# Optimization experiments

Measured on AMD Instinct MI355X. Metric: run time of the kernel, lower is better.

The kernel has to match this reference:

```python
import jax, jax.numpy as jnp
import numpy as np

N = 100000
E = 625000
IN_C, HID_C, OUT_C = 128, 128, 128


def setup_inputs() -> dict:
    key = jax.random.key(0)
    ks = jax.random.split(key, 8)
    x = jax.random.normal(ks[0], (N, IN_C), dtype=jnp.float32)
    edge_index = jax.random.randint(ks[1], (2, E), 0, N, dtype=jnp.int64)
    # SAGEConv layer 1: lin_l (on aggregated neighbors, with bias), lin_r (on root, no bias)
    s1 = 1.0 / np.sqrt(IN_C)
    W1l = jax.random.uniform(ks[2], (HID_C, IN_C), minval=-s1, maxval=s1, dtype=jnp.float32)
    b1l = jax.random.uniform(ks[3], (HID_C,), minval=-s1, maxval=s1, dtype=jnp.float32)
    W1r = jax.random.uniform(ks[4], (HID_C, IN_C), minval=-s1, maxval=s1, dtype=jnp.float32)
    s2 = 1.0 / np.sqrt(HID_C)
    W2l = jax.random.uniform(ks[5], (OUT_C, HID_C), minval=-s2, maxval=s2, dtype=jnp.float32)
    b2l = jax.random.uniform(ks[6], (OUT_C,), minval=-s2, maxval=s2, dtype=jnp.float32)
    W2r = jax.random.uniform(ks[7], (OUT_C, HID_C), minval=-s2, maxval=s2, dtype=jnp.float32)
    return {"x": x, "edge_index": edge_index,
            "W1l": W1l, "b1l": b1l, "W1r": W1r,
            "W2l": W2l, "b2l": b2l, "W2r": W2r}


def _sage_conv(x, src, dst, Wl, bl, Wr, num_nodes):
    # mean aggregation of source features into destination nodes
    agg = jax.ops.segment_sum(x[src], dst, num_segments=num_nodes)  # [N, d]
    cnt = jax.ops.segment_sum(jnp.ones((src.shape[0],), dtype=x.dtype), dst,
                              num_segments=num_nodes)  # [N]
    mean = agg / jnp.maximum(cnt, 1.0)[:, None]  # zero-degree nodes stay 0
    return mean @ Wl.T + bl + x @ Wr.T


def reference(x, edge_index, W1l, b1l, W1r, W2l, b2l, W2r):
    src, dst = edge_index[0], edge_index[1]
    h = jax.nn.sigmoid(_sage_conv(x, src, dst, W1l, b1l, W1r, N))
    out = _sage_conv(h, src, dst, W2l, b2l, W2r, N)
    return out
```

## Files before the change

kernel.cpp:

```cpp
#include <hip/hip_runtime.h>
#include <math.h>

#define NN 100000
#define NE 625000
#define CC 128
#define CAP 32
#define NT 3125

typedef __attribute__((ext_vector_type(8))) short bf16x8;
typedef __attribute__((ext_vector_type(4))) float f32x4;

__device__ __forceinline__ unsigned short f2b(float f) {
    unsigned int u = __float_as_uint(f);
    unsigned int r = (u + 0x7FFFu + ((u >> 16) & 1u)) >> 16;
    return (unsigned short)r;
}
__device__ __forceinline__ float b2f(unsigned int h) {
    return __uint_as_float(h << 16);
}


__global__ void build_kernel(const int* __restrict__ src, const int* __restrict__ dst,
                             int* __restrict__ cnt, int* __restrict__ col) {
    int e = blockIdx.x * blockDim.x + threadIdx.x;
    if (e < NE) {
        int d = dst[e];
        int p = atomicAdd(&cnt[d], 1);
        if (p < CAP) col[d * CAP + p] = src[e];
    }
}


__global__ __launch_bounds__(256) void cvtX_kernel(const float* __restrict__ x,
                                                   unsigned short* __restrict__ xb) {
    size_t i = ((size_t)blockIdx.x * 256 + threadIdx.x) * 4;
    float4 v = *(const float4*)&x[i];
    ushort2 lo = { f2b(v.x), f2b(v.y) };
    ushort2 hi = { f2b(v.z), f2b(v.w) };
    *(ushort2*)&xb[i]     = lo;
    *(ushort2*)&xb[i + 2] = hi;
}


__global__ void cvtW_kernel(const float* __restrict__ W1l, const float* __restrict__ W1r,
                            const float* __restrict__ W2l, const float* __restrict__ W2r,
                            unsigned short* __restrict__ Wcat1,
                            unsigned short* __restrict__ Wcat2) {
    int i = blockIdx.x * blockDim.x + threadIdx.x;
    int layer = i >> 15;
    int local = i & 32767;
    int c = local >> 8;
    int k = local & 255;
    const float* Wl = layer ? W2l : W1l;
    const float* Wr = layer ? W2r : W1r;
    float v = (k < CC) ? Wl[c * CC + k] : Wr[c * CC + (k - CC)];
    (layer ? Wcat2 : Wcat1)[local] = f2b(v);
}


__global__ __launch_bounds__(256) void gather_kernel(const unsigned short* __restrict__ feat,
                                                     const int* __restrict__ cnt,
                                                     const int* __restrict__ col,
                                                     unsigned short* __restrict__ aggb) {
    int gtid = blockIdx.x * blockDim.x + threadIdx.x;
    int node = gtid >> 6;
    if (node >= NN) return;
    int lane = gtid & 63;
    int g    = lane >> 4;
    int c8   = (lane & 15) * 8;
    int deg  = cnt[node];
    int dmin = deg < CAP ? deg : CAP;
    const int* bucket = col + node * CAP;
    float s0 = 0, s1 = 0, s2 = 0, s3 = 0, s4 = 0, s5 = 0, s6 = 0, s7 = 0;
    for (int j = g; j < dmin; j += 4) {
        int s = bucket[j];
        uint4 u = *(const uint4*)&feat[(size_t)s * CC + c8];
        s0 += b2f(u.x & 0xFFFFu); s1 += b2f(u.x >> 16);
        s2 += b2f(u.y & 0xFFFFu); s3 += b2f(u.y >> 16);
        s4 += b2f(u.z & 0xFFFFu); s5 += b2f(u.z >> 16);
        s6 += b2f(u.w & 0xFFFFu); s7 += b2f(u.w >> 16);
    }
    s0 += __shfl_xor(s0, 16); s0 += __shfl_xor(s0, 32);
    s1 += __shfl_xor(s1, 16); s1 += __shfl_xor(s1, 32);
    s2 += __shfl_xor(s2, 16); s2 += __shfl_xor(s2, 32);
    s3 += __shfl_xor(s3, 16); s3 += __shfl_xor(s3, 32);
    s4 += __shfl_xor(s4, 16); s4 += __shfl_xor(s4, 32);
    s5 += __shfl_xor(s5, 16); s5 += __shfl_xor(s5, 32);
    s6 += __shfl_xor(s6, 16); s6 += __shfl_xor(s6, 32);
    s7 += __shfl_xor(s7, 16); s7 += __shfl_xor(s7, 32);
    if (g == 0) {
        float iv = 1.0f / (float)(deg > 0 ? deg : 1);
        uint4 o;
        o.x = (unsigned int)f2b(s0 * iv) | ((unsigned int)f2b(s1 * iv) << 16);
        o.y = (unsigned int)f2b(s2 * iv) | ((unsigned int)f2b(s3 * iv) << 16);
        o.z = (unsigned int)f2b(s4 * iv) | ((unsigned int)f2b(s5 * iv) << 16);
        o.w = (unsigned int)f2b(s6 * iv) | ((unsigned int)f2b(s7 * iv) << 16);
        *(uint4*)&aggb[(size_t)node * CC + c8] = o;
    }
}


__device__ __forceinline__ void load_a_frag(bf16x8 (&a)[2][8],
        const unsigned short* __restrict__ aggb,
        const unsigned short* __restrict__ featb,
        int rt, int m, int kq) {
    const size_t base0 = (size_t)(rt * 32 + m) * CC + kq * 8;
    const size_t base1 = base0 + 16 * CC;
#pragma unroll
    for (int ks = 0; ks < 4; ++ks) {
        a[0][ks]     = *(const bf16x8*)(aggb  + base0 + ks * 32);
        a[1][ks]     = *(const bf16x8*)(aggb  + base1 + ks * 32);
        a[0][4 + ks] = *(const bf16x8*)(featb + base0 + ks * 32);
        a[1][4 + ks] = *(const bf16x8*)(featb + base1 + ks * 32);
    }
}

template<bool SIGMOID, bool OUT_FP32>
__device__ __forceinline__ void compute_store(const bf16x8 (&a)[2][8],
        const bf16x8 (&b)[2][8], int rt, int m, int kq, int col0,
        float bias0, float bias1, void* __restrict__ outv) {
    f32x4 acc[2][2];
#pragma unroll
    for (int r2 = 0; r2 < 2; ++r2)
#pragma unroll
        for (int ct = 0; ct < 2; ++ct) acc[r2][ct] = (f32x4)0.0f;
#pragma unroll
    for (int ks = 0; ks < 8; ++ks) {
#pragma unroll
        for (int ct = 0; ct < 2; ++ct) {
            acc[0][ct] = __builtin_amdgcn_mfma_f32_16x16x32_bf16(a[0][ks], b[ct][ks], acc[0][ct], 0, 0, 0);
            acc[1][ct] = __builtin_amdgcn_mfma_f32_16x16x32_bf16(a[1][ks], b[ct][ks], acc[1][ct], 0, 0, 0);
        }
    }
#pragma unroll
    for (int r2 = 0; r2 < 2; ++r2) {
#pragma unroll
        for (int ct = 0; ct < 2; ++ct) {
            const int c = col0 + ct * 16 + m;
            const float bv = ct ? bias1 : bias0;
#pragma unroll
            for (int i = 0; i < 4; ++i) {
                const int r = rt * 32 + r2 * 16 + kq * 4 + i;
                float v = acc[r2][ct][i] + bv;
                if (SIGMOID) v = 1.0f / (1.0f + __expf(-v));
                if (OUT_FP32) ((float*)outv)[(size_t)r * CC + c] = v;
                else ((unsigned short*)outv)[(size_t)r * CC + c] = f2b(v);
            }
        }
    }
}

template<bool SIGMOID, bool OUT_FP32>
__global__ __launch_bounds__(256, 2) void gemm2_kernel(
        const unsigned short* __restrict__ aggb,
        const unsigned short* __restrict__ featb,
        const unsigned short* __restrict__ Wcat,
        const float* __restrict__ bias,
        void* __restrict__ outv) {
    const int w    = threadIdx.x >> 6;
    const int lane = threadIdx.x & 63;
    const int m    = lane & 15;
    const int kq   = lane >> 4;
    const int col0 = w * 32;

    bf16x8 breg[2][8];
#pragma unroll
    for (int ct = 0; ct < 2; ++ct)
#pragma unroll
        for (int ks = 0; ks < 8; ++ks)
            breg[ct][ks] = *(const bf16x8*)(Wcat + (size_t)(col0 + ct * 16 + m) * 256 + ks * 32 + kq * 8);

    const float bias0 = bias[col0 + m];
    const float bias1 = bias[col0 + 16 + m];

    const int stride = gridDim.x;
    int rt = blockIdx.x;
    if (rt >= NT) return;

    bf16x8 A0[2][8], A1[2][8];
    load_a_frag(A0, aggb, featb, rt, m, kq);
    for (;;) {
        int rt1 = rt + stride;
        if (rt1 < NT) load_a_frag(A1, aggb, featb, rt1, m, kq);
        compute_store<SIGMOID, OUT_FP32>(A0, breg, rt, m, kq, col0, bias0, bias1, outv);
        if (rt1 >= NT) break;
        int rt2 = rt1 + stride;
        if (rt2 < NT) load_a_frag(A0, aggb, featb, rt2, m, kq);
        compute_store<SIGMOID, OUT_FP32>(A1, breg, rt1, m, kq, col0, bias0, bias1, outv);
        if (rt2 >= NT) break;
        rt = rt2;
    }
}


extern "C" void kernel_launch(void* const* d_in, const int* in_sizes, int n_in,
                              void* d_out, int out_size, void* d_ws, size_t ws_size,
                              hipStream_t stream) {
    const float* x   = (const float*)d_in[0];
    const int*   ei  = (const int*)d_in[1];
    const float* W1l = (const float*)d_in[2];
    const float* b1l = (const float*)d_in[3];
    const float* W1r = (const float*)d_in[4];
    const float* W2l = (const float*)d_in[5];
    const float* b2l = (const float*)d_in[6];
    const float* W2r = (const float*)d_in[7];
    float* out = (float*)d_out;

    const int* src = ei;
    const int* dst = ei + NE;

    int* cnt = (int*)d_ws;
    int* col = cnt + NN;
    unsigned short* Wcat1 = (unsigned short*)(col + NN * CAP);
    unsigned short* Wcat2 = Wcat1 + 128 * 256;
    unsigned short* xb    = Wcat2 + 128 * 256;
    unsigned short* aggb  = xb + (size_t)NN * CC;
    unsigned short* hb    = aggb + (size_t)NN * CC;

    hipMemsetAsync(cnt, 0, (size_t)NN * sizeof(int), stream);

    build_kernel<<<(NE + 255) / 256, 256, 0, stream>>>(src, dst, cnt, col);
    cvtX_kernel<<<(NN * CC / 4) / 256, 256, 0, stream>>>(x, xb);
    cvtW_kernel<<<256, 256, 0, stream>>>(W1l, W1r, W2l, W2r, Wcat1, Wcat2);

    const int GB = 512;

    gather_kernel<<<(NN * 64) / 256, 256, 0, stream>>>(xb, cnt, col, aggb);
    gemm2_kernel<true, false><<<GB, 256, 0, stream>>>(aggb, xb, Wcat1, b1l, hb);

    gather_kernel<<<(NN * 64) / 256, 256, 0, stream>>>(hb, cnt, col, aggb);
    gemm2_kernel<false, true><<<GB, 256, 0, stream>>>(aggb, hb, Wcat2, b2l, out);
}
```

Measured before the change: 288.0 us.

## Stage 64-row A tiles through LDS in SAGE GEMM instead of per-wave register loads

Replaces the register-prefetch GEMM, where each wave loaded its own copy of the 32-row A fragments from global memory, with a block-cooperative load of a 64-row concatenated [agg|feat] tile into padded shared memory. All four waves then read their A fragments from LDS. This removes the fourfold redundant global reads of A across waves and doubles rows per tile. It loses the software double-buffering, adds two barriers per tile, and raises the grid size and occupancy target.

```diff
diff --git a/kernel.cpp b/kernel.cpp
--- a/kernel.cpp
+++ b/kernel.cpp
@@ -5,7 +5,8 @@
 #define NE 625000
 #define CC 128
 #define CAP 32
-#define NT 3125
+#define NT2 1563
+#define LSTR 264
 
 typedef __attribute__((ext_vector_type(8))) short bf16x8;
 typedef __attribute__((ext_vector_type(4))) float f32x4;
@@ -100,65 +101,18 @@
 }
 
 
-__device__ __forceinline__ void load_a_frag(bf16x8 (&a)[2][8],
-        const unsigned short* __restrict__ aggb,
-        const unsigned short* __restrict__ featb,
-        int rt, int m, int kq) {
-    const size_t base0 = (size_t)(rt * 32 + m) * CC + kq * 8;
-    const size_t base1 = base0 + 16 * CC;
-#pragma unroll
-    for (int ks = 0; ks < 4; ++ks) {
-        a[0][ks]     = *(const bf16x8*)(aggb  + base0 + ks * 32);
-        a[1][ks]     = *(const bf16x8*)(aggb  + base1 + ks * 32);
-        a[0][4 + ks] = *(const bf16x8*)(featb + base0 + ks * 32);
-        a[1][4 + ks] = *(const bf16x8*)(featb + base1 + ks * 32);
-    }
-}
-
 template<bool SIGMOID, bool OUT_FP32>
-__device__ __forceinline__ void compute_store(const bf16x8 (&a)[2][8],
-        const bf16x8 (&b)[2][8], int rt, int m, int kq, int col0,
-        float bias0, float bias1, void* __restrict__ outv) {
-    f32x4 acc[2][2];
-#pragma unroll
-    for (int r2 = 0; r2 < 2; ++r2)
-#pragma unroll
-        for (int ct = 0; ct < 2; ++ct) acc[r2][ct] = (f32x4)0.0f;
-#pragma unroll
-    for (int ks = 0; ks < 8; ++ks) {
-#pragma unroll
-        for (int ct = 0; ct < 2; ++ct) {
-            acc[0][ct] = __builtin_amdgcn_mfma_f32_16x16x32_bf16(a[0][ks], b[ct][ks], acc[0][ct], 0, 0, 0);
-            acc[1][ct] = __builtin_amdgcn_mfma_f32_16x16x32_bf16(a[1][ks], b[ct][ks], acc[1][ct], 0, 0, 0);
-        }
-    }
-#pragma unroll
-    for (int r2 = 0; r2 < 2; ++r2) {
-#pragma unroll
-        for (int ct = 0; ct < 2; ++ct) {
-            const int c = col0 + ct * 16 + m;
-            const float bv = ct ? bias1 : bias0;
-#pragma unroll
-            for (int i = 0; i < 4; ++i) {
-                const int r = rt * 32 + r2 * 16 + kq * 4 + i;
-                float v = acc[r2][ct][i] + bv;
-                if (SIGMOID) v = 1.0f / (1.0f + __expf(-v));
-                if (OUT_FP32) ((float*)outv)[(size_t)r * CC + c] = v;
-                else ((unsigned short*)outv)[(size_t)r * CC + c] = f2b(v);
-            }
-        }
-    }
-}
-
-template<bool SIGMOID, bool OUT_FP32>
-__global__ __launch_bounds__(256, 2) void gemm2_kernel(
+__global__ __launch_bounds__(256, 3) void gemm3_kernel(
         const unsigned short* __restrict__ aggb,
         const unsigned short* __restrict__ featb,
         const unsigned short* __restrict__ Wcat,
         const float* __restrict__ bias,
         void* __restrict__ outv) {
-    const int w    = threadIdx.x >> 6;
-    const int lane = threadIdx.x & 63;
+    __shared__ unsigned short Acat[64 * LSTR];
+
+    const int t    = threadIdx.x;
+    const int w    = t >> 6;
+    const int lane = t & 63;
     const int m    = lane & 15;
     const int kq   = lane >> 4;
     const int col0 = w * 32;
@@ -173,22 +127,65 @@
     const float bias0 = bias[col0 + m];
     const float bias1 = bias[col0 + 16 + m];
 
-    const int stride = gridDim.x;
-    int rt = blockIdx.x;
-    if (rt >= NT) return;
-
-    bf16x8 A0[2][8], A1[2][8];
-    load_a_frag(A0, aggb, featb, rt, m, kq);
-    for (;;) {
-        int rt1 = rt + stride;
-        if (rt1 < NT) load_a_frag(A1, aggb, featb, rt1, m, kq);
-        compute_store<SIGMOID, OUT_FP32>(A0, breg, rt, m, kq, col0, bias0, bias1, outv);
-        if (rt1 >= NT) break;
-        int rt2 = rt1 + stride;
-        if (rt2 < NT) load_a_frag(A0, aggb, featb, rt2, m, kq);
-        compute_store<SIGMOID, OUT_FP32>(A1, breg, rt1, m, kq, col0, bias0, bias1, outv);
-        if (rt2 >= NT) break;
-        rt = rt2;
+    const int sr  = t >> 2;
+    const int seg = t & 3;
+
+    for (int rt = blockIdx.x; rt < NT2; rt += gridDim.x) {
+        const int row0 = rt * 64;
+
+        int gr = row0 + sr; if (gr >= NN) gr = NN - 1;
+        const unsigned short* srcp = (seg < 2)
+            ? (aggb  + (size_t)gr * CC + seg * 64)
+            : (featb + (size_t)gr * CC + (seg - 2) * 64);
+        bf16x8 st[8];
+#pragma unroll
+        for (int j = 0; j < 8; ++j) st[j] = *(const bf16x8*)(srcp + j * 8);
+
+        __syncthreads();
+
+        unsigned short* q = &Acat[sr * LSTR + seg * 64];
+#pragma unroll
+        for (int j = 0; j < 8; ++j) *(bf16x8*)(q + j * 8) = st[j];
+
+        __syncthreads();
+
+        f32x4 acc[4][2];
+#pragma unroll
+        for (int rt4 = 0; rt4 < 4; ++rt4)
+#pragma unroll
+            for (int ct = 0; ct < 2; ++ct) acc[rt4][ct] = (f32x4)0.0f;
+
+#pragma unroll
+        for (int ks = 0; ks < 8; ++ks) {
+            bf16x8 a[4];
+#pragma unroll
+            for (int rt4 = 0; rt4 < 4; ++rt4)
+                a[rt4] = *(const bf16x8*)&Acat[(rt4 * 16 + m) * LSTR + ks * 32 + kq * 8];
+#pragma unroll
+            for (int rt4 = 0; rt4 < 4; ++rt4) {
+                acc[rt4][0] = __builtin_amdgcn_mfma_f32_16x16x32_bf16(a[rt4], breg[0][ks], acc[rt4][0], 0, 0, 0);
+                acc[rt4][1] = __builtin_amdgcn_mfma_f32_16x16x32_bf16(a[rt4], breg[1][ks], acc[rt4][1], 0, 0, 0);
+            }
+        }
+
+#pragma unroll
+        for (int rt4 = 0; rt4 < 4; ++rt4) {
+#pragma unroll
+            for (int ct = 0; ct < 2; ++ct) {
+                const int c = col0 + ct * 16 + m;
+                const float bv = ct ? bias1 : bias0;
+#pragma unroll
+                for (int i = 0; i < 4; ++i) {
+                    const int r = row0 + rt4 * 16 + kq * 4 + i;
+                    if (r < NN) {
+                        float v = acc[rt4][ct][i] + bv;
+                        if (SIGMOID) v = 1.0f / (1.0f + __expf(-v));
+                        if (OUT_FP32) ((float*)outv)[(size_t)r * CC + c] = v;
+                        else ((unsigned short*)outv)[(size_t)r * CC + c] = f2b(v);
+                    }
+                }
+            }
+        }
     }
 }
 
@@ -223,11 +220,11 @@
     cvtX_kernel<<<(NN * CC / 4) / 256, 256, 0, stream>>>(x, xb);
     cvtW_kernel<<<256, 256, 0, stream>>>(W1l, W1r, W2l, W2r, Wcat1, Wcat2);
 
-    const int GB = 512;
+    const int GB = 1024;
 
     gather_kernel<<<(NN * 64) / 256, 256, 0, stream>>>(xb, cnt, col, aggb);
-    gemm2_kernel<true, false><<<GB, 256, 0, stream>>>(aggb, xb, Wcat1, b1l, hb);
+    gemm3_kernel<true, false><<<GB, 256, 0, stream>>>(aggb, xb, Wcat1, b1l, hb);
 
     gather_kernel<<<(NN * 64) / 256, 256, 0, stream>>>(hb, cnt, col, aggb);
-    gemm2_kernel<false, true><<<GB, 256, 0, stream>>>(aggb, hb, Wcat2, b2l, out);
-}
+    gemm3_kernel<false, true><<<GB, 256, 0, stream>>>(aggb, hb, Wcat2, b2l, out);
+}
```

New measurement: 271.3 us. 1.06x faster.
